# Kernel tuning notes

Hardware: AMD Instinct MI355X
Metric: run time of the kernel (lower is better)

## Reference

```python
import jax, jax.numpy as jnp
import numpy as np

EPS = 1e-5
K = 20

def knn(x, k):
    # x: (B, 3, N) -> idx (B, N, k) of nearest neighbors (negative sq-dist topk)
    inner = -2.0 * jnp.einsum('bcn,bcm->bnm', x, x)
    xx = jnp.sum(x * x, axis=1)  # (B, N)
    pd = -xx[:, :, None] - inner - xx[:, None, :]
    return jax.lax.top_k(pd, k)[1]

def graph_feature(feats, idx):
    # feats: (B, C, N), idx: (B, N, k) -> (B, 2C, N, k)
    ft = jnp.transpose(feats, (0, 2, 1))  # (B, N, C)
    gathered = jax.vmap(lambda f, i: f[i])(ft, idx)  # (B, N, k, C)
    center = ft[:, :, None, :]  # (B, N, 1, C)
    out = jnp.concatenate([gathered - center,
                           jnp.broadcast_to(center, gathered.shape)], axis=3)
    return jnp.transpose(out, (0, 3, 1, 2))  # (B, 2C, N, k)

def bn2d(h, g, b):
    m = jnp.mean(h, axis=(0, 2, 3), keepdims=True)
    v = jnp.var(h, axis=(0, 2, 3), keepdims=True)
    return (h - m) * jax.lax.rsqrt(v + EPS) * g[None, :, None, None] + b[None, :, None, None]

def bn1d(h, g, b):
    m = jnp.mean(h, axis=(0, 2), keepdims=True)
    v = jnp.var(h, axis=(0, 2), keepdims=True)
    return (h - m) * jax.lax.rsqrt(v + EPS) * g[None, :, None] + b[None, :, None]

def edge_block(x, feats, w, g, b):
    idx = knn(x, K)
    ef = graph_feature(feats, idx)                  # (B, 2C, N, k)
    h = jnp.einsum('bcnk,oc->bonk', ef, w)          # 1x1 conv, no bias
    h = jnp.tanh(bn2d(h, g, b))
    return jnp.max(h, axis=-1)                      # (B, O, N)


def setup_inputs() -> dict:
    key = jax.random.key(0)
    ks = jax.random.split(key, 20)
    B, N, FD, EMB = 8, 2048, 3, 1024
    def w_init(k, o, i):
        return jax.random.normal(k, (o, i), dtype=jnp.float32) * (1.0 / np.sqrt(i))
    inp = {
        'x': jax.random.normal(ks[0], (B, N, 3), dtype=jnp.float32),
        'features': jax.random.normal(ks[1], (B, N, FD), dtype=jnp.float32),
        'w1': w_init(ks[2], 64, 2 * FD),
        'g1': jnp.ones((64,), jnp.float32), 'b1': jnp.zeros((64,), jnp.float32),
        'w2': w_init(ks[3], 64, 128),
        'g2': jnp.ones((64,), jnp.float32), 'b2': jnp.zeros((64,), jnp.float32),
        'w3': w_init(ks[4], 128, 128),
        'g3': jnp.ones((128,), jnp.float32), 'b3': jnp.zeros((128,), jnp.float32),
        'w4': w_init(ks[5], 256, 256),
        'g4': jnp.ones((256,), jnp.float32), 'b4': jnp.zeros((256,), jnp.float32),
        'w5': w_init(ks[6], EMB, 512),
        'g5': jnp.ones((EMB,), jnp.float32), 'b5': jnp.zeros((EMB,), jnp.float32),
    }
    return inp


def reference(x, features, w1, g1, b1, w2, g2, b2, w3, g3, b3, w4, g4, b4, w5, g5, b5):
    xt = jnp.transpose(x, (0, 2, 1))          # (B, 3, N)
    ft = jnp.transpose(features, (0, 2, 1))   # (B, FD, N)
    B = xt.shape[0]
    f1 = edge_block(xt, ft, w1, g1, b1)       # (B, 64, N)
    f2 = edge_block(xt, f1, w2, g2, b2)       # (B, 64, N)
    f3 = edge_block(xt, f2, w3, g3, b3)       # (B, 128, N)
    f4 = edge_block(xt, f3, w4, g4, b4)       # (B, 256, N)
    cat = jnp.concatenate([f1, f2, f3, f4], axis=1)   # (B, 512, N)
    f5 = jnp.tanh(bn1d(jnp.einsum('bcn,oc->bon', cat, w5), g5, b5))  # (B, EMB, N)
    mx = jnp.max(f5, axis=-1)
    av = jnp.mean(f5, axis=-1)
    return jnp.concatenate([mx, av], axis=1)  # (B, 2*EMB)
```

## Files before the change

### kernel.cpp

```cpp
#include <hip/hip_runtime.h>
#include <cstdio>
#include <cstdint>

#define NPTS 2048
#define NB   8
#define KK   20

typedef __attribute__((ext_vector_type(8))) short  short8;
typedef __attribute__((ext_vector_type(8))) unsigned short ushort8;
typedef __attribute__((ext_vector_type(4))) float  f32x4;
typedef unsigned short ushort;
typedef unsigned int   uint;

#define AS1 __attribute__((address_space(1)))
#define AS3 __attribute__((address_space(3)))

__device__ __forceinline__ ushort f2bf(float f) {
    uint u = __float_as_uint(f);
    u += 0x7fffu + ((u >> 16) & 1u);
    return (ushort)(u >> 16);
}
__device__ __forceinline__ float bf2f(ushort s) { return __uint_as_float((uint)s << 16); }

__device__ __forceinline__ void gload16(const ushort* g, ushort* l) {
    __builtin_amdgcn_global_load_lds((const AS1 uint*)(const void*)g,
                                     (AS3 uint*)(void*)l, 16, 0, 0);
}

__global__ __launch_bounds__(512) void knn_kernel(const float* __restrict__ x,
                                                  int* __restrict__ idx)
{
    __shared__ float4 sp[NPTS];
    const int tid = threadIdx.x;
    const int wv = tid >> 6, lane = tid & 63;
    const int gn0 = blockIdx.x * 8;
    const int b = gn0 >> 11;
    const float* xb = x + (size_t)b * NPTS * 3;

    for (int p = tid; p < NPTS; p += 512) {
        const float a0 = xb[p * 3 + 0], a1 = xb[p * 3 + 1], a2 = xb[p * 3 + 2];
        sp[p] = make_float4(a0, a1, a2, a0 * a0 + a1 * a1 + a2 * a2);
    }
    __syncthreads();

    const int n = (gn0 & (NPTS - 1)) + wv;
    const float4 pn = sp[n];
    const float xxn = pn.w;

    float d[32];
#pragma unroll
    for (int i = 0; i < 32; ++i) {
        const float4 pm = sp[lane + i * 64];
        const float dot = pm.x * pn.x + pm.y * pn.y + pm.z * pn.z;
        const float inner = -2.0f * dot;
        d[i] = (-xxn - inner) - pm.w;
    }

    float gv[4]; int gs[4];
#pragma unroll
    for (int g = 0; g < 4; ++g) {
        float v = d[g * 8]; int s = 0;
#pragma unroll
        for (int j = 1; j < 8; ++j)
            if (d[g * 8 + j] > v) { v = d[g * 8 + j]; s = j; }
        gv[g] = v; gs[g] = s;
    }

    int* op = idx + ((size_t)b * NPTS + n) * KK;
    for (int it = 0; it < KK; ++it) {
        float bv = gv[0]; int bm8 = gs[0];
#pragma unroll
        for (int g = 1; g < 4; ++g)
            if (gv[g] > bv) { bv = gv[g]; bm8 = g * 8 + gs[g]; }
        const int m = lane + (bm8 << 6);

        const uint u = __float_as_uint(bv);
        const uint r = (u & 0x80000000u) ? ~u : (u | 0x80000000u);
        unsigned long long key =
            ((unsigned long long)r << 11) | (unsigned)(2047 - m);

#pragma unroll
        for (int s2 = 32; s2; s2 >>= 1) {
            const unsigned long long ok =
                (unsigned long long)__shfl_xor((long long)key, s2);
            key = (ok > key) ? ok : key;
        }
        const int mw = 2047 - (int)(key & 2047u);
        if (lane == 0) op[it] = mw;

        const int mws   = __builtin_amdgcn_readfirstlane(mw);
        const int wslot = mws >> 6;
        const int wgrp  = wslot >> 3;
        const int wj    = wslot & 7;
        const bool iswin = (lane == (mws & 63));

#pragma unroll
        for (int G = 0; G < 4; ++G) {
            if (wgrp == G) {
#pragma unroll
                for (int j = 0; j < 8; ++j)
                    if (j == wj) d[G * 8 + j] = iswin ? -1e38f : d[G * 8 + j];
                float v = d[G * 8]; int s = 0;
#pragma unroll
                for (int j = 1; j < 8; ++j)
                    if (d[G * 8 + j] > v) { v = d[G * 8 + j]; s = j; }
                gv[G] = v; gs[G] = s;
            }
        }
    }
}

__global__ __launch_bounds__(256) void y1_kernel(const float* __restrict__ feats,
                                                 const float* __restrict__ w1,
                                                 float* __restrict__ Y)
{
    __shared__ float w[384];
    const int tid = threadIdx.x;
    for (int i = tid; i < 384; i += 256) w[i] = w1[i];
    __syncthreads();

    const int b  = blockIdx.y;
    const int p  = blockIdx.x * 2 + (tid >> 7);
    const int o2 = tid & 127;
    const int o = o2 & 63, half = o2 >> 6;
    const float* fp = feats + ((size_t)b * NPTS + p) * 3;
    const float f0 = fp[0], f1 = fp[1], f2 = fp[2];
    const float* wr = &w[o * 6 + half * 3];
    Y[((size_t)b * NPTS + p) * 128 + o2] = wr[0] * f0 + wr[1] * f1 + wr[2] * f2;
}

__global__ __launch_bounds__(256) void wsplit_kernel(const float* __restrict__ w2,
                                                     const float* __restrict__ w3,
                                                     const float* __restrict__ w4,
                                                     ushort* q2h, ushort* q2l,
                                                     ushort* q3h, ushort* q3l,
                                                     ushort* q4h, ushort* q4l)
{
    const int t = blockIdx.x * 256 + threadIdx.x;
    float v; ushort *dh, *dl; int off;
    if (t < 8192)        { int i = t;         int m = i >> 6, c = i & 63;  int o = m & 63,  hf = m >> 6; v = w2[o * 128 + hf * 64  + c]; dh = q2h; dl = q2l; off = i; }
    else if (t < 24576)  { int i = t - 8192;  int m = i >> 6, c = i & 63;  int o = m & 127, hf = m >> 7; v = w3[o * 128 + hf * 64  + c]; dh = q3h; dl = q3l; off = i; }
    else if (t < 90112)  { int i = t - 24576; int m = i >> 7, c = i & 127; int o = m & 255, hf = m >> 8; v = w4[o * 256 + hf * 128 + c]; dh = q4h; dl = q4l; off = i; }
    else return;
    const ushort h = f2bf(v);
    dh[off] = h;
    dl[off] = f2bf(v - bf2f(h));
}

template<bool PF32>
__global__ __launch_bounds__(256) void gemm_mfma(const float* __restrict__ Pf,
                                                 const ushort* __restrict__ Ph,
                                                 const ushort* __restrict__ Pl,
                                                 const ushort* __restrict__ Qh,
                                                 const ushort* __restrict__ Ql,
                                                 float* __restrict__ Out,
                                                 int K, int pitchP, int pitchQ, int ldO,
                                                 long strideP, long strideQ, long strideO)
{
    constexpr int PH = 0, PL = 8192, QH = 16384, QL = 24576;
    __shared__ ushort lds_buf[32768];

    const int tid  = threadIdx.x;
    const int wv   = tid >> 6, lane = tid & 63;
    const int i0   = blockIdx.x * 128;
    const int j0   = blockIdx.y * 128;
    const long prow0 = (long)blockIdx.z * strideP + (long)i0 * pitchP;
    const long qrow0 = (long)blockIdx.z * strideQ + (long)j0 * pitchQ;

    const int iw = (wv >> 1) * 64;
    const int jw = (wv & 1) * 64;
    const int lr = lane & 15;
    const int lc = lane >> 4;

    f32x4 acc[4][4];
#pragma unroll
    for (int f = 0; f < 4; ++f)
#pragma unroll
        for (int g = 0; g < 4; ++g) acc[f][g] = (f32x4){0.f, 0.f, 0.f, 0.f};

    for (int k0 = 0; k0 < K; k0 += 64) {
        __syncthreads();
        {
            const int r8 = lane >> 3;
            const int cp = lane & 7;
#pragma unroll
            for (int q = 0; q < 4; ++q) {
                const int row = wv * 32 + q * 8 + r8;
                const int cl  = cp ^ (row & 7);
                const long go = (long)row * pitchQ + k0 + cl * 8;
                gload16(Qh + qrow0 + go, &lds_buf[QH + (wv * 32 + q * 8) * 64]);
                gload16(Ql + qrow0 + go, &lds_buf[QL + (wv * 32 + q * 8) * 64]);
            }
        }
        if constexpr (!PF32) {
            const int r8 = lane >> 3;
            const int cp = lane & 7;
#pragma unroll
            for (int q = 0; q < 4; ++q) {
                const int row = wv * 32 + q * 8 + r8;
                const int cl  = cp ^ (row & 7);
                const long go = (long)row * pitchP + k0 + cl * 8;
                gload16(Ph + prow0 + go, &lds_buf[PH + (wv * 32 + q * 8) * 64]);
                gload16(Pl + prow0 + go, &lds_buf[PL + (wv * 32 + q * 8) * 64]);
            }
        } else {
#pragma unroll
            for (int r = 0; r < 4; ++r) {
                const int id  = r * 256 + tid;
                const int row = id >> 3, cl = id & 7;
                const int cp  = cl ^ (row & 7);
                const float* gp = Pf + prow0 + (long)row * pitchP + k0 + cl * 8;
                const float4 v0 = *(const float4*)gp;
                const float4 v1 = *(const float4*)(gp + 4);
                const float vv[8] = {v0.x, v0.y, v0.z, v0.w, v1.x, v1.y, v1.z, v1.w};
                ushort8 hi, lo;
#pragma unroll
                for (int e2 = 0; e2 < 8; ++e2) {
                    const ushort h = f2bf(vv[e2]);
                    hi[e2] = h;
                    lo[e2] = f2bf(vv[e2] - bf2f(h));
                }
                *(ushort8*)&lds_buf[PH + row * 64 + cp * 8] = hi;
                *(ushort8*)&lds_buf[PL + row * 64 + cp * 8] = lo;
            }
        }
        asm volatile("s_waitcnt vmcnt(0)" ::: "memory");
        __syncthreads();

#pragma unroll
        for (int kk = 0; kk < 2; ++kk) {
            const int cpa = (kk * 4 + lc) ^ (lr & 7);
            short8 ah[4], al[4], bh[4], bl[4];
#pragma unroll
            for (int f = 0; f < 4; ++f) {
                const int ra = (iw + f * 16 + lr) * 64 + cpa * 8;
                ah[f] = *(const short8*)&lds_buf[PH + ra];
                al[f] = *(const short8*)&lds_buf[PL + ra];
                const int rb = (jw + f * 16 + lr) * 64 + cpa * 8;
                bh[f] = *(const short8*)&lds_buf[QH + rb];
                bl[f] = *(const short8*)&lds_buf[QL + rb];
            }
#pragma unroll
            for (int f = 0; f < 4; ++f)
#pragma unroll
                for (int g = 0; g < 4; ++g) {
                    acc[f][g] = __builtin_amdgcn_mfma_f32_16x16x32_bf16(ah[f], bh[g], acc[f][g], 0, 0, 0);
                    acc[f][g] = __builtin_amdgcn_mfma_f32_16x16x32_bf16(ah[f], bl[g], acc[f][g], 0, 0, 0);
                    acc[f][g] = __builtin_amdgcn_mfma_f32_16x16x32_bf16(al[f], bh[g], acc[f][g], 0, 0, 0);
                }
        }
    }

    const long ob = (long)blockIdx.z * strideO;
#pragma unroll
    for (int f = 0; f < 4; ++f) {
        const int i = i0 + iw + f * 16 + lc * 4;
#pragma unroll
        for (int g = 0; g < 4; ++g) {
            const int j = j0 + jw + g * 16 + lr;
#pragma unroll
            for (int r = 0; r < 4; ++r)
                Out[ob + (long)(i + r) * ldO + j] = acc[f][g][r];
        }
    }
}

template<int O, int NCH>
__global__ __launch_bounds__(256) void edge_apply(const float* __restrict__ Y,
                                                  const int* __restrict__ knn_idx,
                                                  float* __restrict__ mx_out,
                                                  double* __restrict__ st)
{
    constexpr int M = 2 * O;
    constexpr int NPB = 256 / O;
    const int blk = blockIdx.x;
    const int b     = blk & 7;
    const int chunk = blk >> 3;
    const int tid = threadIdx.x;
    const int o   = tid & (O - 1);
    const int sub = tid / O;
    const int n0  = chunk * (NPB * NCH);
    const size_t rowb = (size_t)b * NPTS;
    float s = 0.f, s2 = 0.f;

#pragma unroll
    for (int it = 0; it < NCH; ++it) {
        const int n = n0 + it * NPB + sub;
        const float* yr = Y + (rowb + n) * M;
        const float base = yr[O + o] - yr[o];
        const int* ip = knn_idx + (rowb + n) * KK;
        int mm[KK];
#pragma unroll
        for (int j = 0; j < KK; ++j) mm[j] = ip[j];
        float h[KK];
#pragma unroll
        for (int j = 0; j < KK; ++j) h[j] = Y[(rowb + mm[j]) * M + o];
        float mx = -1e38f;
#pragma unroll
        for (int j = 0; j < KK; ++j) {
            const float v = h[j] + base;
            mx = fmaxf(mx, v);
            s += v;
            s2 = fmaf(v, v, s2);
        }
        mx_out[(rowb + n) * O + o] = mx;
    }
    double* stp = st + (size_t)(chunk & 7) * (2 * O);
    atomicAdd(&stp[o],     (double)s);
    atomicAdd(&stp[O + o], (double)s2);
}

template<int O>
__global__ __launch_bounds__(256) void edge_finalize(const float* __restrict__ mx_in,
                                                     const double* __restrict__ st,
                                                     const float* __restrict__ gamma,
                                                     const float* __restrict__ beta,
                                                     ushort* __restrict__ ch,
                                                     ushort* __restrict__ cl_,
                                                     int c0)
{
    __shared__ float ssc[256], ssh[256];
    const int b = blockIdx.y;
    const int tid = threadIdx.x;
    if (tid < O) {
        double ssum = 0.0, s2sum = 0.0;
#pragma unroll
        for (int sl = 0; sl < 8; ++sl) {
            ssum  += st[(size_t)sl * (2 * O) + tid];
            s2sum += st[(size_t)sl * (2 * O) + O + tid];
        }
        const double cnt = (double)NB * NPTS * KK;
        const double mean = ssum / cnt;
        const double var  = s2sum / cnt - mean * mean;
        const float rs = rsqrtf((float)var + 1e-5f);
        const float sc = gamma[tid] * rs;
        ssc[tid] = sc;
        ssh[tid] = beta[tid] - (float)mean * sc;
    }
    __syncthreads();

    const int o   = tid & (O - 1);
    const int sub = tid / O;
    const int n0  = blockIdx.x * 8;
    constexpr int NPB = 256 / O;
#pragma unroll
    for (int it = 0; it < 8 / NPB; ++it) {
        const int n = n0 + it * NPB + sub;
        const float v = mx_in[((size_t)b * NPTS + n) * O + o];
        const float f = tanhf(fmaf(v, ssc[o], ssh[o]));
        const ushort h = f2bf(f);
        const size_t co = ((size_t)b * NPTS + n) * 512 + c0 + o;
        ch[co]  = h;
        cl_[co] = f2bf(f - bf2f(h));
    }
}

__global__ __launch_bounds__(256) void estats_kernel(const float* __restrict__ e,
                                                     double* __restrict__ st)
{
    const int o = blockIdx.x;
    const int tid = threadIdx.x;
    double s = 0.0, s2 = 0.0;
    for (int b = 0; b < NB; ++b) {
        const float* row = e + ((size_t)(b * 1024 + o)) * NPTS;
        for (int n = tid; n < NPTS; n += 256) {
            const float v = row[n];
            s  += v;
            s2 += (double)v * v;
        }
    }
    __shared__ double sh_s[4], sh_s2[4];
#pragma unroll
    for (int d = 32; d > 0; d >>= 1) { s += __shfl_xor(s, d); s2 += __shfl_xor(s2, d); }
    const int lane = tid & 63, wv = tid >> 6;
    if (lane == 0) { sh_s[wv] = s; sh_s2[wv] = s2; }
    __syncthreads();
    if (tid == 0) {
        st[o]        = sh_s[0] + sh_s[1] + sh_s[2] + sh_s[3];
        st[1024 + o] = sh_s2[0] + sh_s2[1] + sh_s2[2] + sh_s2[3];
    }
}

__global__ __launch_bounds__(256) void final_kernel(const float* __restrict__ e,
                                                    const double* __restrict__ st,
                                                    const float* __restrict__ g5,
                                                    const float* __restrict__ b5,
                                                    float* __restrict__ out)
{
    const int b = blockIdx.y;
    const int wv = threadIdx.x >> 6, lane = threadIdx.x & 63;
    const int o = blockIdx.x * 4 + wv;
    const double cnt = (double)NB * NPTS;
    const double mean = st[o] / cnt;
    const double var  = st[1024 + o] / cnt - mean * mean;
    const float rs = rsqrtf((float)var + 1e-5f);
    const float sc = g5[o] * rs;
    const float sh = b5[o] - (float)mean * sc;
    const float* row = e + ((size_t)(b * 1024 + o)) * NPTS;
    float mx = -1e38f, sm = 0.f;
    for (int n = lane; n < NPTS; n += 64) {
        const float v = tanhf(fmaf(row[n], sc, sh));
        mx = fmaxf(mx, v);
        sm += v;
    }
#pragma unroll
    for (int d = 32; d > 0; d >>= 1) {
        mx = fmaxf(mx, __shfl_xor(mx, d));
        sm += __shfl_xor(sm, d);
    }
    if (lane == 0) {
        out[(size_t)b * 2048 + o]        = mx;
        out[(size_t)b * 2048 + 1024 + o] = sm * (1.0f / 2048.0f);
    }
}

extern "C" void kernel_launch(void* const* d_in, const int* in_sizes, int n_in,
                              void* d_out, int out_size, void* d_ws, size_t ws_size,
                              hipStream_t stream)
{
    (void)in_sizes; (void)n_in; (void)out_size;
    const float* x  = (const float*)d_in[0];
    const float* ft = (const float*)d_in[1];
    const float* w1 = (const float*)d_in[2];
    const float* g1 = (const float*)d_in[3];
    const float* b1 = (const float*)d_in[4];
    const float* w2 = (const float*)d_in[5];
    const float* g2 = (const float*)d_in[6];
    const float* b2 = (const float*)d_in[7];
    const float* w3 = (const float*)d_in[8];
    const float* g3 = (const float*)d_in[9];
    const float* b3 = (const float*)d_in[10];
    const float* w4 = (const float*)d_in[11];
    const float* g4 = (const float*)d_in[12];
    const float* b4 = (const float*)d_in[13];
    const float* w5 = (const float*)d_in[14];
    const float* g5 = (const float*)d_in[15];
    const float* b5 = (const float*)d_in[16];
    float* out = (float*)d_out;

    const size_t STATS_OFF = 0;
    const size_t ESTAT_OFF = 131072;
    const size_t IDX_OFF   = 147456;
    const size_t Q2H_OFF   = 1458176,  Q2L_OFF = 1474560;
    const size_t Q3H_OFF   = 1490944,  Q3L_OFF = 1523712;
    const size_t Q4H_OFF   = 1556480,  Q4L_OFF = 1687552;
    const size_t CTH_OFF   = 1835008;
    const size_t CTL_OFF   = 18612224;
    const size_t Y_OFF     = 35389440;
    const size_t MX_OFF    = 68943872;
    const size_t NEED      = 102498304;
    if (ws_size < NEED) {
        fprintf(stderr, "kernel_launch: ws too small (%zu < %zu)\n", ws_size, NEED);
        return;
    }
    char* ws = (char*)d_ws;
    double* stats  = (double*)(ws + STATS_OFF);
    double* estats = (double*)(ws + ESTAT_OFF);
    int*    idx    = (int*)(ws + IDX_OFF);
    ushort* q2h = (ushort*)(ws + Q2H_OFF); ushort* q2l = (ushort*)(ws + Q2L_OFF);
    ushort* q3h = (ushort*)(ws + Q3H_OFF); ushort* q3l = (ushort*)(ws + Q3L_OFF);
    ushort* q4h = (ushort*)(ws + Q4H_OFF); ushort* q4l = (ushort*)(ws + Q4L_OFF);
    ushort* cth = (ushort*)(ws + CTH_OFF); ushort* ctl = (ushort*)(ws + CTL_OFF);
    float*  Y   = (float*)(ws + Y_OFF);
    float*  mxb = (float*)(ws + MX_OFF);
    float*  e   = (float*)(ws + Y_OFF);

    hipMemsetAsync(stats, 0, 131072, stream);

    knn_kernel<<<NB * NPTS / 8, 512, 0, stream>>>(x, idx);
    wsplit_kernel<<<352, 256, 0, stream>>>(w2, w3, w4, q2h, q2l, q3h, q3l, q4h, q4l);

    y1_kernel<<<dim3(NPTS / 2, NB), 256, 0, stream>>>(ft, w1, Y);
    edge_apply<64, 2><<<2048, 256, 0, stream>>>(Y, idx, mxb, stats + 0 * 4096);
    edge_finalize<64><<<dim3(256, NB), 256, 0, stream>>>(mxb, stats + 0 * 4096, g1, b1, cth, ctl, 0);

    gemm_mfma<false><<<dim3(16, 1, 8), 256, 0, stream>>>(
        nullptr, cth + 0, ctl + 0, q2h, q2l, Y,
        64, 512, 64, 128, (long)NPTS * 512, 0, (long)NPTS * 128);
    edge_apply<64, 2><<<2048, 256, 0, stream>>>(Y, idx, mxb, stats + 1 * 4096);
    edge_finalize<64><<<dim3(256, NB), 256, 0, stream>>>(mxb, stats + 1 * 4096, g2, b2, cth, ctl, 64);

    gemm_mfma<false><<<dim3(16, 2, 8), 256, 0, stream>>>(
        nullptr, cth + 64, ctl + 64, q3h, q3l, Y,
        64, 512, 64, 256, (long)NPTS * 512, 0, (long)NPTS * 256);
    edge_apply<128, 4><<<2048, 256, 0, stream>>>(Y, idx, mxb, stats + 2 * 4096);
    edge_finalize<128><<<dim3(256, NB), 256, 0, stream>>>(mxb, stats + 2 * 4096, g3, b3, cth, ctl, 128);

    gemm_mfma<false><<<dim3(16, 4, 8), 256, 0, stream>>>(
        nullptr, cth + 128, ctl + 128, q4h, q4l, Y,
        128, 512, 128, 512, (long)NPTS * 512, 0, (long)NPTS * 512);
    edge_apply<256, 8><<<2048, 256, 0, stream>>>(Y, idx, mxb, stats + 3 * 4096);
    edge_finalize<256><<<dim3(256, NB), 256, 0, stream>>>(mxb, stats + 3 * 4096, g4, b4, cth, ctl, 256);

    gemm_mfma<true><<<dim3(8, 16, 8), 256, 0, stream>>>(
        w5, nullptr, nullptr, cth, ctl, e,
        512, 512, 512, 2048, 0, (long)NPTS * 512, (long)1024 * 2048);
    estats_kernel<<<1024, 256, 0, stream>>>(e, estats);
    final_kernel<<<dim3(256, NB), 256, 0, stream>>>(e, estats, g5, b5, out);
}
```

Baseline: 400.7 us.

## Fuse final BN statistics into last GEMM epilogue, pre-split w5, swizzle block order

The separate estats pass that re-read the 64 MB final GEMM output is removed; per-channel sum and sum-of-squares are now reduced in the GEMM epilogue with shuffles and double atomics into 8 slabs, which final_kernel sums. w5 is optionally pre-split into bf16 hi/lo once when the workspace is large enough, avoiding per-tile fp32 conversion. Blocks of the last GEMM are launched on a 1D grid with a swizzled order to improve L2 reuse. The cost is atomic traffic in the epilogue, a larger workspace, and a fallback path when the workspace is too small.

```diff
diff --git a/kernel.cpp b/kernel.cpp
--- a/kernel.cpp
+++ b/kernel.cpp
@@ -147,13 +147,25 @@
     dl[off] = f2bf(v - bf2f(h));
 }
 
-template<bool PF32>
+__global__ __launch_bounds__(256) void wsplit5_kernel(const float* __restrict__ w5,
+                                                      ushort* q5h, ushort* q5l)
+{
+    const int t = blockIdx.x * 256 + threadIdx.x;
+    if (t >= 1024 * 512) return;
+    const float v = w5[t];
+    const ushort h = f2bf(v);
+    q5h[t] = h;
+    q5l[t] = f2bf(v - bf2f(h));
+}
+
+template<bool PF32, bool STATS, bool SWZ>
 __global__ __launch_bounds__(256) void gemm_mfma(const float* __restrict__ Pf,
                                                  const ushort* __restrict__ Ph,
                                                  const ushort* __restrict__ Pl,
                                                  const ushort* __restrict__ Qh,
                                                  const ushort* __restrict__ Ql,
                                                  float* __restrict__ Out,
+                                                 double* __restrict__ est,
                                                  int K, int pitchP, int pitchQ, int ldO,
                                                  long strideP, long strideQ, long strideO)
 {
@@ -162,10 +174,18 @@
 
     const int tid  = threadIdx.x;
     const int wv   = tid >> 6, lane = tid & 63;
-    const int i0   = blockIdx.x * 128;
-    const int j0   = blockIdx.y * 128;
-    const long prow0 = (long)blockIdx.z * strideP + (long)i0 * pitchP;
-    const long qrow0 = (long)blockIdx.z * strideQ + (long)j0 * pitchQ;
+
+    int bx, by, bz;
+    if constexpr (SWZ) {
+        const int id = blockIdx.x;
+        const int J  = (id & 7) * 128 + (id >> 3);
+        bx = J & 7; by = (J >> 3) & 15; bz = J >> 7;
+    } else { bx = blockIdx.x; by = blockIdx.y; bz = blockIdx.z; }
+
+    const int i0   = bx * 128;
+    const int j0   = by * 128;
+    const long prow0 = (long)bz * strideP + (long)i0 * pitchP;
+    const long qrow0 = (long)bz * strideQ + (long)j0 * pitchQ;
 
     const int iw = (wv >> 1) * 64;
     const int jw = (wv & 1) * 64;
@@ -251,7 +271,7 @@
         }
     }
 
-    const long ob = (long)blockIdx.z * strideO;
+    const long ob = (long)bz * strideO;
 #pragma unroll
     for (int f = 0; f < 4; ++f) {
         const int i = i0 + iw + f * 16 + lc * 4;
@@ -262,6 +282,32 @@
             for (int r = 0; r < 4; ++r)
                 Out[ob + (long)(i + r) * ldO + j] = acc[f][g][r];
         }
+    }
+
+    if constexpr (STATS) {
+        const int slab = (by + bz) & 7;
+#pragma unroll
+        for (int f = 0; f < 4; ++f)
+#pragma unroll
+            for (int r = 0; r < 4; ++r) {
+                float s = 0.f, s2 = 0.f;
+#pragma unroll
+                for (int g = 0; g < 4; ++g) {
+                    const float v = acc[f][g][r];
+                    s += v;
+                    s2 = fmaf(v, v, s2);
+                }
+#pragma unroll
+                for (int d2 = 1; d2 <= 8; d2 <<= 1) {
+                    s  += __shfl_xor(s, d2);
+                    s2 += __shfl_xor(s2, d2);
+                }
+                if (lr == 0) {
+                    const int i = i0 + iw + f * 16 + lc * 4 + r;
+                    atomicAdd(&est[(size_t)slab * 2048 + i],        (double)s);
+                    atomicAdd(&est[(size_t)slab * 2048 + 1024 + i], (double)s2);
+                }
+            }
     }
 }
 
@@ -355,32 +401,6 @@
     }
 }
 
-__global__ __launch_bounds__(256) void estats_kernel(const float* __restrict__ e,
-                                                     double* __restrict__ st)
-{
-    const int o = blockIdx.x;
-    const int tid = threadIdx.x;
-    double s = 0.0, s2 = 0.0;
-    for (int b = 0; b < NB; ++b) {
-        const float* row = e + ((size_t)(b * 1024 + o)) * NPTS;
-        for (int n = tid; n < NPTS; n += 256) {
-            const float v = row[n];
-            s  += v;
-            s2 += (double)v * v;
-        }
-    }
-    __shared__ double sh_s[4], sh_s2[4];
-#pragma unroll
-    for (int d = 32; d > 0; d >>= 1) { s += __shfl_xor(s, d); s2 += __shfl_xor(s2, d); }
-    const int lane = tid & 63, wv = tid >> 6;
-    if (lane == 0) { sh_s[wv] = s; sh_s2[wv] = s2; }
-    __syncthreads();
-    if (tid == 0) {
-        st[o]        = sh_s[0] + sh_s[1] + sh_s[2] + sh_s[3];
-        st[1024 + o] = sh_s2[0] + sh_s2[1] + sh_s2[2] + sh_s2[3];
-    }
-}
-
 __global__ __launch_bounds__(256) void final_kernel(const float* __restrict__ e,
                                                     const double* __restrict__ st,
                                                     const float* __restrict__ g5,
@@ -390,9 +410,15 @@
     const int b = blockIdx.y;
     const int wv = threadIdx.x >> 6, lane = threadIdx.x & 63;
     const int o = blockIdx.x * 4 + wv;
+    double ssum = 0.0, s2sum = 0.0;
+#pragma unroll
+    for (int sl = 0; sl < 8; ++sl) {
+        ssum  += st[(size_t)sl * 2048 + o];
+        s2sum += st[(size_t)sl * 2048 + 1024 + o];
+    }
     const double cnt = (double)NB * NPTS;
-    const double mean = st[o] / cnt;
-    const double var  = st[1024 + o] / cnt - mean * mean;
+    const double mean = ssum / cnt;
+    const double var  = s2sum / cnt - mean * mean;
     const float rs = rsqrtf((float)var + 1e-5f);
     const float sc = g5[o] * rs;
     const float sh = b5[o] - (float)mean * sc;
@@ -440,19 +466,23 @@
 
     const size_t STATS_OFF = 0;
     const size_t ESTAT_OFF = 131072;
-    const size_t IDX_OFF   = 147456;
-    const size_t Q2H_OFF   = 1458176,  Q2L_OFF = 1474560;
-    const size_t Q3H_OFF   = 1490944,  Q3L_OFF = 1523712;
-    const size_t Q4H_OFF   = 1556480,  Q4L_OFF = 1687552;
-    const size_t CTH_OFF   = 1835008;
-    const size_t CTL_OFF   = 18612224;
-    const size_t Y_OFF     = 35389440;
-    const size_t MX_OFF    = 68943872;
-    const size_t NEED      = 102498304;
-    if (ws_size < NEED) {
-        fprintf(stderr, "kernel_launch: ws too small (%zu < %zu)\n", ws_size, NEED);
+    const size_t IDX_OFF   = 262144;
+    const size_t Q2H_OFF   = 1572864,  Q2L_OFF = 1589248;
+    const size_t Q3H_OFF   = 1605632,  Q3L_OFF = 1638400;
+    const size_t Q4H_OFF   = 1671168,  Q4L_OFF = 1802240;
+    const size_t CTH_OFF   = 1933312;
+    const size_t CTL_OFF   = 18710528;
+    const size_t Y_OFF     = 35487744;
+    const size_t MX_OFF    = 69042176;
+    const size_t NEED_BASE = 102596608;
+    const size_t Q5H_OFF   = 102596608, Q5L_OFF = 103645184;
+    const size_t NEED_FULL = 104693760;
+    if (ws_size < NEED_BASE) {
+        fprintf(stderr, "kernel_launch: ws too small (%zu < %zu)\n", ws_size, NEED_BASE);
         return;
     }
+    const bool presplit = (ws_size >= NEED_FULL);
+
     char* ws = (char*)d_ws;
     double* stats  = (double*)(ws + STATS_OFF);
     double* estats = (double*)(ws + ESTAT_OFF);
@@ -460,41 +490,49 @@
     ushort* q2h = (ushort*)(ws + Q2H_OFF); ushort* q2l = (ushort*)(ws + Q2L_OFF);
     ushort* q3h = (ushort*)(ws + Q3H_OFF); ushort* q3l = (ushort*)(ws + Q3L_OFF);
     ushort* q4h = (ushort*)(ws + Q4H_OFF); ushort* q4l = (ushort*)(ws + Q4L_OFF);
+    ushort* q5h = (ushort*)(ws + Q5H_OFF); ushort* q5l = (ushort*)(ws + Q5L_OFF);
     ushort* cth = (ushort*)(ws + CTH_OFF); ushort* ctl = (ushort*)(ws + CTL_OFF);
     float*  Y   = (float*)(ws + Y_OFF);
     float*  mxb = (float*)(ws + MX_OFF);
     float*  e   = (float*)(ws + Y_OFF);
 
-    hipMemsetAsync(stats, 0, 131072, stream);
+    hipMemsetAsync(ws, 0, 262144, stream);
 
     knn_kernel<<<NB * NPTS / 8, 512, 0, stream>>>(x, idx);
     wsplit_kernel<<<352, 256, 0, stream>>>(w2, w3, w4, q2h, q2l, q3h, q3l, q4h, q4l);
+    if (presplit)
+        wsplit5_kernel<<<2048, 256, 0, stream>>>(w5, q5h, q5l);
 
     y1_kernel<<<dim3(NPTS / 2, NB), 256, 0, stream>>>(ft, w1, Y);
     edge_apply<64, 2><<<2048, 256, 0, stream>>>(Y, idx, mxb, stats + 0 * 4096);
     edge_finalize<64><<<dim3(256, NB), 256, 0, stream>>>(mxb, stats + 0 * 4096, g1, b1, cth, ctl, 0);
 
-    gemm_mfma<false><<<dim3(16, 1, 8), 256, 0, stream>>>(
-        nullptr, cth + 0, ctl + 0, q2h, q2l, Y,
+    gemm_mfma<false, false, false><<<dim3(16, 1, 8), 256, 0, stream>>>(
+        nullptr, cth + 0, ctl + 0, q2h, q2l, Y, nullptr,
         64, 512, 64, 128, (long)NPTS * 512, 0, (long)NPTS * 128);
     edge_apply<64, 2><<<2048, 256, 0, stream>>>(Y, idx, mxb, stats + 1 * 4096);
     edge_finalize<64><<<dim3(256, NB), 256, 0, stream>>>(mxb, stats + 1 * 4096, g2, b2, cth, ctl, 64);
 
-    gemm_mfma<false><<<dim3(16, 2, 8), 256, 0, stream>>>(
-        nullptr, cth + 64, ctl + 64, q3h, q3l, Y,
+    gemm_mfma<false, false, false><<<dim3(16, 2, 8), 256, 0, stream>>>(
+        nullptr, cth + 64, ctl + 64, q3h, q3l, Y, nullptr,
         64, 512, 64, 256, (long)NPTS * 512, 0, (long)NPTS * 256);
     edge_apply<128, 4><<<2048, 256, 0, stream>>>(Y, idx, mxb, stats + 2 * 4096);
     edge_finalize<128><<<dim3(256, NB), 256, 0, stream>>>(mxb, stats + 2 * 4096, g3, b3, cth, ctl, 128);
 
-    gemm_mfma<false><<<dim3(16, 4, 8), 256, 0, stream>>>(
-        nullptr, cth + 128, ctl + 128, q4h, q4l, Y,
+    gemm_mfma<false, false, false><<<dim3(16, 4, 8), 256, 0, stream>>>(
+        nullptr, cth + 128, ctl + 128, q4h, q4l, Y, nullptr,
         128, 512, 128, 512, (long)NPTS * 512, 0, (long)NPTS * 512);
     edge_apply<256, 8><<<2048, 256, 0, stream>>>(Y, idx, mxb, stats + 3 * 4096);
     edge_finalize<256><<<dim3(256, NB), 256, 0, stream>>>(mxb, stats + 3 * 4096, g4, b4, cth, ctl, 256);
 
-    gemm_mfma<true><<<dim3(8, 16, 8), 256, 0, stream>>>(
-        w5, nullptr, nullptr, cth, ctl, e,
-        512, 512, 512, 2048, 0, (long)NPTS * 512, (long)1024 * 2048);
-    estats_kernel<<<1024, 256, 0, stream>>>(e, estats);
+    if (presplit) {
+        gemm_mfma<false, true, true><<<1024, 256, 0, stream>>>(
+            nullptr, q5h, q5l, cth, ctl, e, estats,
+            512, 512, 512, 2048, 0, (long)NPTS * 512, (long)1024 * 2048);
+    } else {
+        gemm_mfma<true, true, true><<<1024, 256, 0, stream>>>(
+            w5, nullptr, nullptr, cth, ctl, e, estats,
+            512, 512, 512, 2048, 0, (long)NPTS * 512, (long)1024 * 2048);
+    }
     final_kernel<<<dim3(256, NB), 256, 0, stream>>>(e, estats, g5, b5, out);
 }
```

Result: faster. 376.7 us (-6.0%).
